# Kernel tuning notes

Hardware: AMD Instinct MI355X
Metric: run time of the kernel (lower is better)

The kernel has to match this reference:

```python
import jax, jax.numpy as jnp
import numpy as np

HID, E, S, L_CAP, EPS = 768, 1536, 128, 512, 1e-5


def _rope_seq(x):
    """RoPE along axis 1. x: [b, n, 2, s]."""
    n, s = x.shape[1], x.shape[-1]
    half = s // 2
    inv_freq = jnp.power(10000.0, -jnp.arange(half, dtype=x.dtype) / half)  # [half]
    sinusoid = jnp.arange(n, dtype=x.dtype)[:, None, None] * inv_freq       # [n,1,half]
    sin, cos = jnp.sin(sinusoid), jnp.cos(sinusoid)
    x1, x2 = jnp.split(x, 2, axis=-1)
    return jnp.concatenate([x1 * cos - x2 * sin, x2 * cos + x1 * sin], axis=-1)


def setup_inputs() -> dict:
    key = jax.random.key(0)
    ks = jax.random.split(key, 6)
    B, L = 32, 512
    return {
        "x": jax.random.normal(ks[0], (B, L, HID), dtype=jnp.float32),
        "ln_gamma": jnp.ones((HID,), jnp.float32),
        "ln_beta": jnp.zeros((HID,), jnp.float32),
        "uv_W": jax.random.normal(ks[1], (HID, 2 * E + S), jnp.float32) * 0.02,
        "uv_b": jnp.zeros((2 * E + S,), jnp.float32),
        "gamma_qk": jax.random.normal(ks[2], (2, S), jnp.float32) * 0.02,
        "beta_qk": jnp.zeros((2, S), jnp.float32),
        "w_rel": jax.random.normal(ks[3], (2 * L_CAP - 1,), jnp.float32) * 0.02,
        "o_W": jax.random.normal(ks[4], (E, HID), jnp.float32) * 0.02,
        "o_b": jnp.zeros((HID,), jnp.float32),
    }


def reference(x, ln_gamma, ln_beta, uv_W, uv_b, gamma_qk, beta_qk, w_rel, o_W, o_b):
    L = x.shape[1]
    shortcut = x
    # LayerNorm
    mu = jnp.mean(x, axis=-1, keepdims=True)
    var = jnp.mean(jnp.square(x - mu), axis=-1, keepdims=True)
    xn = (x - mu) * jax.lax.rsqrt(var + EPS) * ln_gamma + ln_beta
    # uv projection + silu, split into u, v, base
    uv = jax.nn.silu(xn @ uv_W + uv_b)                       # [b, n, 2e+s]
    u, v, base = jnp.split(uv, [E, 2 * E], axis=-1)          # [b,n,e], [b,n,e], [b,n,s]
    # per-head affine then RoPE -> q, k
    base = base[..., None, :] * gamma_qk + beta_qk           # [b, n, 2, s]
    base = _rope_seq(base)
    q, k = base[..., 0, :], base[..., 1, :]
    # relu^2 attention kernel with Toeplitz relative position bias
    qk = jnp.einsum('bnd,bmd->bnm', q, k)
    idx = jnp.arange(L)
    bias = w_rel[idx[None, :] - idx[:, None] + L - 1]        # bias[i,j] = w[j-i+L-1]
    kernel = jnp.square(jax.nn.relu(qk / L + bias))
    # gated value aggregation + output projection + residual
    out = u * jnp.einsum('bnm,bme->bne', kernel, v)
    out = out @ o_W + o_b
    return out + shortcut
```

## Files before the change

kernel.cpp:

```cpp
#include <hip/hip_runtime.h>
#include <hip/hip_bf16.h>
#include <math.h>

typedef __bf16 bf16x8 __attribute__((ext_vector_type(8)));
typedef float f32x4 __attribute__((ext_vector_type(4)));
typedef unsigned short u16x4 __attribute__((ext_vector_type(4)));

#define AS1P const __attribute__((address_space(1))) void*
#define AS3P __attribute__((address_space(3))) void*

__device__ __forceinline__ float b2f(unsigned short h) {
    unsigned int u = ((unsigned int)h) << 16;
    return __builtin_bit_cast(float, u);
}
__device__ __forceinline__ unsigned short f2b(float f) {
    unsigned int u = __builtin_bit_cast(unsigned int, f);
    u += 0x7FFFu + ((u >> 16) & 1u);
    return (unsigned short)(u >> 16);
}
__device__ __forceinline__ float silu(float c) {
    return c * __builtin_amdgcn_rcpf(1.0f + __expf(-c));
}

__global__ __launch_bounds__(256) void k_convT(const float* __restrict__ src,
                                               unsigned short* __restrict__ dst,
                                               int R, int C) {
    __shared__ float tile[32][33];
    int tx = threadIdx.x, ty = threadIdx.y;
    int r0 = blockIdx.y << 5, c0 = blockIdx.x << 5;
#pragma unroll
    for (int i = 0; i < 4; ++i)
        tile[ty + 8 * i][tx] = src[(long long)(r0 + ty + 8 * i) * C + c0 + tx];
    __syncthreads();
#pragma unroll
    for (int i = 0; i < 4; ++i)
        dst[(long long)(c0 + ty + 8 * i) * R + r0 + tx] = f2b(tile[tx][ty + 8 * i]);
}

__global__ __launch_bounds__(256) void k_ln(const float* __restrict__ x,
                                            const float* __restrict__ g,
                                            const float* __restrict__ b,
                                            unsigned short* __restrict__ xn) {
    int row = blockIdx.x;
    int t = threadIdx.x;
    const float* xr = x + (long long)row * 768;
    float v0 = xr[t], v1 = xr[t + 256], v2 = xr[t + 512];
    float s = v0 + v1 + v2;
    float q = v0 * v0 + v1 * v1 + v2 * v2;
#pragma unroll
    for (int off = 32; off > 0; off >>= 1) {
        s += __shfl_xor(s, off);
        q += __shfl_xor(q, off);
    }
    __shared__ float ss[4], sq[4];
    int w = t >> 6;
    if ((t & 63) == 0) { ss[w] = s; sq[w] = q; }
    __syncthreads();
    float S_ = ss[0] + ss[1] + ss[2] + ss[3];
    float Q_ = sq[0] + sq[1] + sq[2] + sq[3];
    float mu = S_ * (1.0f / 768.0f);
    float var = Q_ * (1.0f / 768.0f) - mu * mu;
    float rs = rsqrtf(var + 1e-5f);
    unsigned short* xo = xn + (long long)row * 768;
    xo[t]       = f2b((v0 - mu) * rs * g[t]       + b[t]);
    xo[t + 256] = f2b((v1 - mu) * rs * g[t + 256] + b[t + 256]);
    xo[t + 512] = f2b((v2 - mu) * rs * g[t + 512] + b[t + 512]);
}

__global__ __launch_bounds__(128) void k_rope(const unsigned short* __restrict__ bS,
                                              const float* __restrict__ gqk,
                                              const float* __restrict__ bqk,
                                              unsigned short* __restrict__ q,
                                              unsigned short* __restrict__ k) {
    int row = blockIdx.x;
    int l = row & 511;
    int s = threadIdx.x;
    int j = s & 63;
    int partner = s ^ 64;
    float b0 = b2f(bS[(long long)row * 128 + s]);
    float bp = b2f(bS[(long long)row * 128 + partner]);
    float invf = __expf((float)j * -0.14391156831f);
    float th = (float)l * invf;
    float sn, cs;
    __sincosf(th, &sn, &cs);
    float sign = (s < 64) ? -1.0f : 1.0f;
    float preq  = b0 * gqk[s]           + bqk[s];
    float preqp = bp * gqk[partner]     + bqk[partner];
    q[(long long)row * 128 + s] = f2b(preq * cs + sign * preqp * sn);
    float prek  = b0 * gqk[128 + s]       + bqk[128 + s];
    float prekp = bp * gqk[128 + partner] + bqk[128 + partner];
    k[(long long)row * 128 + s] = f2b(prek * cs + sign * prekp * sn);
}

template <int EPI, int K>
__global__ __launch_bounds__(256) void k_g2(const unsigned short* __restrict__ A,
                                            const unsigned short* __restrict__ B,
                                            const float* __restrict__ p1,
                                            unsigned short* __restrict__ out_) {
    __shared__ __align__(16) unsigned short As[128 * 64];
    __shared__ __align__(16) unsigned short Bs[128 * 64];
    int t = threadIdx.x;
    int w = t >> 6, lane = t & 63;
    int wr = w >> 1, wc = w & 1;
    int bx = blockIdx.x, by = blockIdx.y, bz = blockIdx.z;
    {
        int gx = gridDim.x, gy = gridDim.y;
        int nb = gx * gy * gridDim.z;
        int bid = (bz * gy + by) * gx + bx;
        int s = (bid & 7) * (nb >> 3) + (bid >> 3);
        bx = s % gx;
        by = (s / gx) % gy;
        bz = s / (gx * gy);
    }
    const unsigned short* Ab;
    const unsigned short* Bb;
    if constexpr (EPI == 1) {
        Ab = A + (long long)bz * 512 * 128 + (long long)by * 128 * 128;
        Bb = B + (long long)bz * 512 * 128 + (long long)bx * 128 * 128;
    } else {
        Ab = A + (long long)by * 128 * 768;
        Bb = B;
    }

    f32x4 acc[4][4];
#pragma unroll
    for (int m = 0; m < 4; ++m)
#pragma unroll
        for (int n = 0; n < 4; ++n) acc[m][n] = (f32x4){0.f, 0.f, 0.f, 0.f};

    int rowA = (w << 3) + (lane >> 3);
    int colA = (lane & 7) << 3;

    for (int k0 = 0; k0 < K; k0 += 64) {
#pragma unroll
        for (int i = 0; i < 4; ++i) {
            int r = (i << 5) + rowA;
            __builtin_amdgcn_global_load_lds(
                (AS1P)(Ab + (long long)r * K + k0 + colA),
                (AS3P)(&As[(i << 11) + (w << 9)]), 16, 0, 0);
            __builtin_amdgcn_global_load_lds(
                (AS1P)(Bb + (long long)r * K + k0 + colA),
                (AS3P)(&Bs[(i << 11) + (w << 9)]), 16, 0, 0);
        }
        __syncthreads();
#pragma unroll
        for (int ks = 0; ks < 2; ++ks) {
            bf16x8 af[4], bfr[4];
#pragma unroll
            for (int m = 0; m < 4; ++m)
                af[m] = *(const bf16x8*)&As[((wr << 6) + (m << 4) + (lane & 15)) * 64 +
                                            (ks << 5) + ((lane >> 4) << 3)];
#pragma unroll
            for (int n = 0; n < 4; ++n)
                bfr[n] = *(const bf16x8*)&Bs[((wc << 6) + (n << 4) + (lane & 15)) * 64 +
                                             (ks << 5) + ((lane >> 4) << 3)];
#pragma unroll
            for (int m = 0; m < 4; ++m)
#pragma unroll
                for (int n = 0; n < 4; ++n)
                    acc[m][n] = __builtin_amdgcn_mfma_f32_16x16x32_bf16(bfr[n], af[m],
                                                                        acc[m][n], 0, 0, 0);
        }
        __syncthreads();
    }

    int c15 = lane & 15, qq = lane >> 4;
    int rowb = (by << 7) + (wr << 6) + c15;
    int colb = (bx << 7) + (wc << 6) + (qq << 2);
#pragma unroll
    for (int m = 0; m < 4; ++m) {
#pragma unroll
        for (int n = 0; n < 4; ++n) {
            int grow = rowb + (m << 4);
            int gcol = colb + (n << 4);
            f32x4 a = acc[m][n];
            u16x4 o;
            if constexpr (EPI == 1) {
                int base = gcol - grow + 511;
#pragma unroll
                for (int i = 0; i < 4; ++i) {
                    float val = a[i] * (1.0f / 512.0f) + p1[base + i];
                    val = fmaxf(val, 0.0f);
                    o[i] = f2b(val * val);
                }
                *(u16x4*)(out_ + ((long long)(bz * 512 + grow)) * 512 + gcol) = o;
            } else {
#pragma unroll
                for (int i = 0; i < 4; ++i)
                    o[i] = f2b(silu(a[i] + p1[gcol + i]));
                *(u16x4*)(out_ + (long long)grow * 128 + gcol) = o;
            }
        }
    }
}

__device__ __forceinline__ bf16x8 ldsread(const unsigned short* p) {
    bf16x8 r;
    unsigned int off =
        (unsigned int)(unsigned long long)(__attribute__((address_space(3))) const void*)p;
    asm volatile("ds_read_b128 %0, %1" : "=v"(r) : "v"(off));
    return r;
}
__device__ __forceinline__ void stage_half(const unsigned short* __restrict__ g, int ldk,
                                           unsigned short* lds, int t) {
#pragma unroll
    for (int i = 0; i < 2; ++i) {
        int slot = t + (i << 9);
        int row = slot >> 2;
        int gs = (slot & 3) ^ ((slot >> 3) & 3);
        __builtin_amdgcn_global_load_lds(
            (AS1P)(g + (long long)row * ldk + (gs << 3)),
            (AS3P)(lds + slot * 8), 16, 0, 0);
    }
}

template <bool SWAP, int NT, int NF>
__device__ __forceinline__ void kloop8(const unsigned short* __restrict__ Ab,
                                       const unsigned short* __restrict__ Bb,
                                       unsigned short* As, unsigned short* Bs,
                                       f32x4 (&acc)[8][NF], int tid,
                                       int wr, int wc, int c15, int qq, int gq) {
    constexpr int K = NT * 64;
    stage_half(Ab, K, As + 0, tid);
    stage_half(Bb, K, Bs + 0, tid);
    stage_half(Ab + 32, K, As + 8192, tid);
    stage_half(Bb + 32, K, Bs + 8192, tid);
    stage_half(Ab + 64, K, As + 16384, tid);
    stage_half(Bb + 64, K, Bs + 16384, tid);
    asm volatile("s_waitcnt vmcnt(8)" ::: "memory");
    __builtin_amdgcn_s_barrier();

    bf16x8 bfr[NF], af[4];
    for (int t = 0; t < NT; ++t) {
        const int b = t & 1;
        const unsigned short* A0 = As + b * 16384;
        const unsigned short* B0 = Bs + b * 16384;
#pragma unroll
        for (int p = 0; p < 4; ++p) {
            const int ks = p >> 1, mh = p & 1;
            const unsigned short* At = A0 + ks * 8192;
            const unsigned short* Bt = B0 + ks * 8192;
            if (mh == 0) {
#pragma unroll
                for (int n = 0; n < NF; ++n)
                    bfr[n] = ldsread(Bt + (wc * (NF * 16) + n * 16 + c15) * 32 + gq * 8);
            }
#pragma unroll
            for (int j = 0; j < 4; ++j)
                af[j] = ldsread(At + (wr * 128 + (mh * 4 + j) * 16 + c15) * 32 + gq * 8);
            if (p == 0) {
                if (t + 1 < NT)
                    stage_half(Ab + (t + 1) * 64 + 32, K,
                               As + (((t + 1) & 1) * 2 + 1) * 8192, tid);
            } else if (p == 1) {
                if (t + 1 < NT)
                    stage_half(Bb + (t + 1) * 64 + 32, K,
                               Bs + (((t + 1) & 1) * 2 + 1) * 8192, tid);
            } else if (p == 2) {
                if (t + 2 < NT)
                    stage_half(Ab + (t + 2) * 64, K, As + (b * 2) * 8192, tid);
            } else {
                if (t + 2 < NT)
                    stage_half(Bb + (t + 2) * 64, K, Bs + (b * 2) * 8192, tid);
            }
            __builtin_amdgcn_s_barrier();
            asm volatile("s_waitcnt lgkmcnt(0)" ::: "memory");
            __builtin_amdgcn_sched_barrier(0);
            __builtin_amdgcn_s_setprio(1);
#pragma unroll
            for (int j = 0; j < 4; ++j)
#pragma unroll
                for (int n = 0; n < NF; ++n) {
                    if constexpr (SWAP)
                        acc[mh * 4 + j][n] = __builtin_amdgcn_mfma_f32_16x16x32_bf16(
                            bfr[n], af[j], acc[mh * 4 + j][n], 0, 0, 0);
                    else
                        acc[mh * 4 + j][n] = __builtin_amdgcn_mfma_f32_16x16x32_bf16(
                            af[j], bfr[n], acc[mh * 4 + j][n], 0, 0, 0);
                }
            __builtin_amdgcn_s_setprio(0);
            if (p == 1) {
                if (t < NT - 1)
                    asm volatile("s_waitcnt vmcnt(8)" ::: "memory");
                else
                    asm volatile("s_waitcnt vmcnt(0)" ::: "memory");
            } else if (p == 3) {
                if (t < NT - 2)
                    asm volatile("s_waitcnt vmcnt(8)" ::: "memory");
                else if (t == NT - 2)
                    asm volatile("s_waitcnt vmcnt(4)" ::: "memory");
            }
            __builtin_amdgcn_sched_barrier(0);
            __builtin_amdgcn_s_barrier();
        }
    }
}

template <int EPI, int SWZ, int NT, int NF>
__global__ __launch_bounds__(512, 2) void k8(const unsigned short* __restrict__ A,
                                             const unsigned short* __restrict__ B,
                                             long long strideA, long long strideB,
                                             void* p0, void* p1, void* p2,
                                             const void* p3) {
    constexpr int K = NT * 64;
    __shared__ __align__(16) unsigned short As[2][2][256 * 32];
    __shared__ __align__(16) unsigned short Bs[2][2][256 * 32];
    int tid = threadIdx.x;
    int w = tid >> 6, lane = tid & 63;
    int wr = w >> 2, wc = w & 3;
    int c15 = lane & 15, qq = lane >> 4;
    int gq = qq ^ ((c15 >> 1) & 3);
    int bx = blockIdx.x, by = blockIdx.y, bz = blockIdx.z;
    if constexpr (SWZ == 1) {
        int gx = gridDim.x;
        int nb = gx * gridDim.y;
        int bid = by * gx + bx;
        int s = (bid & 7) * (nb >> 3) + (bid >> 3);
        bx = s % gx;
        by = s / gx;
    } else if constexpr (SWZ == 2) {
        int gx = gridDim.x, gy = gridDim.y;
        int nb = gx * gy * gridDim.z;
        int bid = (bz * gy + by) * gx + bx;
        int s = (bid & 7) * (nb >> 3) + (bid >> 3);
        bx = s % gx;
        by = (s / gx) % gy;
        bz = s / (gx * gy);
    }
    const unsigned short* Ab = A + bz * strideA + (long long)by * 256 * K;
    const unsigned short* Bb = B + bz * strideB + (long long)bx * (NF * 64) * K;

    f32x4 acc[8][NF];
#pragma unroll
    for (int m = 0; m < 8; ++m)
#pragma unroll
        for (int n = 0; n < NF; ++n) acc[m][n] = (f32x4){0.f, 0.f, 0.f, 0.f};

    bool swapped = true;
    if constexpr (EPI == 10) {
        swapped = (bx < 6);
        if (swapped)
            kloop8<true, NT, NF>(Ab, Bb, &As[0][0][0], &Bs[0][0][0], acc, tid, wr, wc, c15, qq, gq);
        else
            kloop8<false, NT, NF>(Ab, Bb, &As[0][0][0], &Bs[0][0][0], acc, tid, wr, wc, c15, qq, gq);
    } else {
        kloop8<true, NT, NF>(Ab, Bb, &As[0][0][0], &Bs[0][0][0], acc, tid, wr, wc, c15, qq, gq);
    }

    if constexpr (EPI == 10) {
        if (swapped) {
            int rowb = by * 256 + wr * 128 + c15;
            int colb = bx * 256 + wc * 64 + (qq << 2);
#pragma unroll
            for (int m = 0; m < 8; ++m) {
#pragma unroll
                for (int n = 0; n < NF; ++n) {
                    int R = rowb + m * 16;
                    int C = colb + n * 16;
                    f32x4 a = acc[m][n];
                    f32x4 bb = *(const f32x4*)((const float*)p3 + C);
                    u16x4 o;
#pragma unroll
                    for (int i = 0; i < 4; ++i) o[i] = f2b(silu(a[i] + bb[i]));
                    *(u16x4*)((unsigned short*)p0 + (long long)R * 1536 + C) = o;
                }
            }
        } else {
            int rowb = by * 256 + wr * 128 + (qq << 2);
            int colb = bx * 256 + wc * 64 + c15;
#pragma unroll
            for (int m = 0; m < 8; ++m) {
#pragma unroll
                for (int n = 0; n < NF; ++n) {
                    int R = rowb + m * 16;
                    int C = colb + n * 16;
                    float bias = ((const float*)p3)[C];
                    f32x4 a = acc[m][n];
                    u16x4 o;
#pragma unroll
                    for (int i = 0; i < 4; ++i) o[i] = f2b(silu(a[i] + bias));
                    int bb2 = R >> 9, mm = R & 511;
                    *(u16x4*)((unsigned short*)p1 +
                              ((long long)bb2 * 1600 + (C - 1536)) * 512 + mm) = o;
                }
            }
        }
    } else if constexpr (EPI == 2) {
        int rowb = by * 256 + wr * 128 + c15;
        int colb = bx * (NF * 64) + wc * (NF * 16) + (qq << 2);
#pragma unroll
        for (int m = 0; m < 8; ++m) {
#pragma unroll
            for (int n = 0; n < NF; ++n) {
                int R = rowb + m * 16;
                int C = colb + n * 16;
                f32x4 a = acc[m][n];
                long long idx = ((long long)(bz * 512 + R)) * 1536 + C;
                u16x4 uu = *(const u16x4*)((const unsigned short*)p1 + idx);
                u16x4 o;
#pragma unroll
                for (int i = 0; i < 4; ++i) o[i] = f2b(a[i] * b2f(uu[i]));
                *(u16x4*)((unsigned short*)p0 + idx) = o;
            }
        }
    } else {
        int rowb = by * 256 + wr * 128 + c15;
        int colb = bx * (NF * 64) + wc * (NF * 16) + (qq << 2);
#pragma unroll
        for (int m = 0; m < 8; ++m) {
#pragma unroll
            for (int n = 0; n < NF; ++n) {
                int R = rowb + m * 16;
                int C = colb + n * 16;
                f32x4 a = acc[m][n];
                long long idx = (long long)R * 768 + C;
                f32x4 xv = *(const f32x4*)((const float*)p2 + idx);
                f32x4 ob = *(const f32x4*)((const float*)p1 + C);
                f32x4 o;
#pragma unroll
                for (int i = 0; i < 4; ++i) o[i] = a[i] + ob[i] + xv[i];
                *(f32x4*)((float*)p0 + idx) = o;
            }
        }
    }
}

extern "C" void kernel_launch(void* const* d_in, const int* in_sizes, int n_in,
                              void* d_out, int out_size, void* d_ws, size_t ws_size,
                              hipStream_t stream) {
    const float* x     = (const float*)d_in[0];
    const float* ln_g  = (const float*)d_in[1];
    const float* ln_b  = (const float*)d_in[2];
    const float* uv_W  = (const float*)d_in[3];
    const float* uv_b  = (const float*)d_in[4];
    const float* g_qk  = (const float*)d_in[5];
    const float* b_qk  = (const float*)d_in[6];
    const float* w_rel = (const float*)d_in[7];
    const float* o_W   = (const float*)d_in[8];
    const float* o_b   = (const float*)d_in[9];
    float* out = (float*)d_out;

    char* ws = (char*)d_ws;
    size_t off = 0;
    auto alloc = [&](size_t bytes) {
        void* p = ws + off;
        off += (bytes + 255) & ~(size_t)255;
        return p;
    };
    unsigned short* uvWT = (unsigned short*)alloc(3200ll * 768 * 2);
    unsigned short* oWT  = (unsigned short*)alloc(832ll * 1536 * 2);
    unsigned short* xn   = (unsigned short*)alloc(16384ll * 768 * 2);
    unsigned short* u    = (unsigned short*)alloc(16384ll * 1536 * 2);
    unsigned short* vT   = (unsigned short*)alloc(32ll * 1600 * 512 * 2);
    unsigned short* bS   = (unsigned short*)alloc(16384ll * 128 * 2);
    unsigned short* q    = (unsigned short*)alloc(32ll * 512 * 128 * 2);
    unsigned short* k    = (unsigned short*)alloc(32ll * 512 * 128 * 2);
    unsigned short* P     = xn;
    unsigned short* gated = u;

    k_convT<<<dim3(100, 24), dim3(32, 8), 0, stream>>>(uv_W, uvWT, 768, 3200);
    k_convT<<<dim3(24, 48), dim3(32, 8), 0, stream>>>(o_W, oWT, 1536, 768);
    k_ln<<<16384, 256, 0, stream>>>(x, ln_g, ln_b, xn);
    k8<10, 1, 12, 4><<<dim3(12, 64), 512, 0, stream>>>(
        xn, uvWT, 0, 0, (void*)u, (void*)vT, nullptr, (const void*)uv_b);
    k_g2<5, 768><<<dim3(1, 128), 256, 0, stream>>>(
        xn, uvWT + 3072ll * 768, uv_b + 3072, bS);
    k_rope<<<16384, 128, 0, stream>>>(bS, g_qk, b_qk, q, k);
    k_g2<1, 128><<<dim3(4, 4, 32), 256, 0, stream>>>(q, k, w_rel, P);
    k8<2, 2, 8, 3><<<dim3(8, 2, 32), 512, 0, stream>>>(
        P, vT, 512ll * 512, 1600ll * 512, (void*)gated, (void*)u, nullptr, nullptr);
    k8<3, 1, 24, 3><<<dim3(4, 64), 512, 0, stream>>>(
        gated, oWT, 0, 0, (void*)out, (void*)o_b, (void*)x, nullptr);
}
```

Baseline: 273.6 us.

## Retile base projection to 64-row blocks and move QK scores onto k8 kernel

The small base-projection GEMM (N=128) is now a dedicated kernel with 64-row tiles, which doubles the grid to 256 blocks for better CU occupancy. The q·k^T relu² score GEMM moves from the 128x128-tile k_g2 kernel to the larger pipelined k8 kernel with a new EPI==1 epilogue that applies the Toeplitz bias. The k buffer is padded by 128 rows, presumably so the k8 loads may read past the end safely. The trade is fewer blocks for the score GEMM (256 vs 512) against the better pipelining in k8.

```diff
diff --git a/kernel.cpp b/kernel.cpp
--- a/kernel.cpp
+++ b/kernel.cpp
@@ -92,70 +92,56 @@
     k[(long long)row * 128 + s] = f2b(prek * cs + sign * prekp * sn);
 }
 
-template <int EPI, int K>
-__global__ __launch_bounds__(256) void k_g2(const unsigned short* __restrict__ A,
+__global__ __launch_bounds__(256) void k_bs(const unsigned short* __restrict__ A,
                                             const unsigned short* __restrict__ B,
-                                            const float* __restrict__ p1,
+                                            const float* __restrict__ bias,
                                             unsigned short* __restrict__ out_) {
-    __shared__ __align__(16) unsigned short As[128 * 64];
+    __shared__ __align__(16) unsigned short As[64 * 64];
     __shared__ __align__(16) unsigned short Bs[128 * 64];
     int t = threadIdx.x;
     int w = t >> 6, lane = t & 63;
     int wr = w >> 1, wc = w & 1;
-    int bx = blockIdx.x, by = blockIdx.y, bz = blockIdx.z;
-    {
-        int gx = gridDim.x, gy = gridDim.y;
-        int nb = gx * gy * gridDim.z;
-        int bid = (bz * gy + by) * gx + bx;
-        int s = (bid & 7) * (nb >> 3) + (bid >> 3);
-        bx = s % gx;
-        by = (s / gx) % gy;
-        bz = s / (gx * gy);
-    }
-    const unsigned short* Ab;
-    const unsigned short* Bb;
-    if constexpr (EPI == 1) {
-        Ab = A + (long long)bz * 512 * 128 + (long long)by * 128 * 128;
-        Bb = B + (long long)bz * 512 * 128 + (long long)bx * 128 * 128;
-    } else {
-        Ab = A + (long long)by * 128 * 768;
-        Bb = B;
-    }
-
-    f32x4 acc[4][4];
-#pragma unroll
-    for (int m = 0; m < 4; ++m)
+    int by = blockIdx.x;
+    const unsigned short* Ab = A + (long long)by * 64 * 768;
+
+    f32x4 acc[2][4];
+#pragma unroll
+    for (int m = 0; m < 2; ++m)
 #pragma unroll
         for (int n = 0; n < 4; ++n) acc[m][n] = (f32x4){0.f, 0.f, 0.f, 0.f};
 
     int rowA = (w << 3) + (lane >> 3);
     int colA = (lane & 7) << 3;
 
-    for (int k0 = 0; k0 < K; k0 += 64) {
+    for (int k0 = 0; k0 < 768; k0 += 64) {
+#pragma unroll
+        for (int i = 0; i < 2; ++i) {
+            int r = (i << 5) + rowA;
+            __builtin_amdgcn_global_load_lds(
+                (AS1P)(Ab + (long long)r * 768 + k0 + colA),
+                (AS3P)(&As[(i << 11) + (w << 9)]), 16, 0, 0);
+        }
 #pragma unroll
         for (int i = 0; i < 4; ++i) {
             int r = (i << 5) + rowA;
             __builtin_amdgcn_global_load_lds(
-                (AS1P)(Ab + (long long)r * K + k0 + colA),
-                (AS3P)(&As[(i << 11) + (w << 9)]), 16, 0, 0);
-            __builtin_amdgcn_global_load_lds(
-                (AS1P)(Bb + (long long)r * K + k0 + colA),
+                (AS1P)(B + (long long)r * 768 + k0 + colA),
                 (AS3P)(&Bs[(i << 11) + (w << 9)]), 16, 0, 0);
         }
         __syncthreads();
 #pragma unroll
         for (int ks = 0; ks < 2; ++ks) {
-            bf16x8 af[4], bfr[4];
-#pragma unroll
-            for (int m = 0; m < 4; ++m)
-                af[m] = *(const bf16x8*)&As[((wr << 6) + (m << 4) + (lane & 15)) * 64 +
+            bf16x8 af[2], bfr[4];
+#pragma unroll
+            for (int m = 0; m < 2; ++m)
+                af[m] = *(const bf16x8*)&As[((wr << 5) + (m << 4) + (lane & 15)) * 64 +
                                             (ks << 5) + ((lane >> 4) << 3)];
 #pragma unroll
             for (int n = 0; n < 4; ++n)
                 bfr[n] = *(const bf16x8*)&Bs[((wc << 6) + (n << 4) + (lane & 15)) * 64 +
                                              (ks << 5) + ((lane >> 4) << 3)];
 #pragma unroll
-            for (int m = 0; m < 4; ++m)
+            for (int m = 0; m < 2; ++m)
 #pragma unroll
                 for (int n = 0; n < 4; ++n)
                     acc[m][n] = __builtin_amdgcn_mfma_f32_16x16x32_bf16(bfr[n], af[m],
@@ -165,31 +151,20 @@
     }
 
     int c15 = lane & 15, qq = lane >> 4;
-    int rowb = (by << 7) + (wr << 6) + c15;
-    int colb = (bx << 7) + (wc << 6) + (qq << 2);
-#pragma unroll
-    for (int m = 0; m < 4; ++m) {
+    int rowb = (by << 6) + (wr << 5) + c15;
+    int colb = (wc << 6) + (qq << 2);
+#pragma unroll
+    for (int m = 0; m < 2; ++m) {
 #pragma unroll
         for (int n = 0; n < 4; ++n) {
             int grow = rowb + (m << 4);
             int gcol = colb + (n << 4);
             f32x4 a = acc[m][n];
             u16x4 o;
-            if constexpr (EPI == 1) {
-                int base = gcol - grow + 511;
-#pragma unroll
-                for (int i = 0; i < 4; ++i) {
-                    float val = a[i] * (1.0f / 512.0f) + p1[base + i];
-                    val = fmaxf(val, 0.0f);
-                    o[i] = f2b(val * val);
-                }
-                *(u16x4*)(out_ + ((long long)(bz * 512 + grow)) * 512 + gcol) = o;
-            } else {
-#pragma unroll
-                for (int i = 0; i < 4; ++i)
-                    o[i] = f2b(silu(a[i] + p1[gcol + i]));
-                *(u16x4*)(out_ + (long long)grow * 128 + gcol) = o;
-            }
+#pragma unroll
+            for (int i = 0; i < 4; ++i)
+                o[i] = f2b(silu(a[i] + bias[gcol + i]));
+            *(u16x4*)(out_ + (long long)grow * 128 + gcol) = o;
         }
     }
 }
@@ -385,6 +360,28 @@
                 }
             }
         }
+    } else if constexpr (EPI == 1) {
+        const float* wrel = (const float*)p1;
+        int rowb = by * 256 + wr * 128 + c15;
+        int colb = bx * (NF * 64) + wc * (NF * 16) + (qq << 2);
+#pragma unroll
+        for (int m = 0; m < 8; ++m) {
+#pragma unroll
+            for (int n = 0; n < NF; ++n) {
+                int R = rowb + m * 16;
+                int C = colb + n * 16;
+                f32x4 a = acc[m][n];
+                int base = C - R + 511;
+                u16x4 o;
+#pragma unroll
+                for (int i = 0; i < 4; ++i) {
+                    float val = a[i] * (1.0f / 512.0f) + wrel[base + i];
+                    val = fmaxf(val, 0.0f);
+                    o[i] = f2b(val * val);
+                }
+                *(u16x4*)((unsigned short*)p0 + ((long long)(bz * 512 + R)) * 512 + C) = o;
+            }
+        }
     } else if constexpr (EPI == 2) {
         int rowb = by * 256 + wr * 128 + c15;
         int colb = bx * (NF * 64) + wc * (NF * 16) + (qq << 2);
@@ -454,7 +451,7 @@
     unsigned short* vT   = (unsigned short*)alloc(32ll * 1600 * 512 * 2);
     unsigned short* bS   = (unsigned short*)alloc(16384ll * 128 * 2);
     unsigned short* q    = (unsigned short*)alloc(32ll * 512 * 128 * 2);
-    unsigned short* k    = (unsigned short*)alloc(32ll * 512 * 128 * 2);
+    unsigned short* k    = (unsigned short*)alloc((32ll * 512 + 128) * 128 * 2);
     unsigned short* P     = xn;
     unsigned short* gated = u;
 
@@ -463,10 +460,10 @@
     k_ln<<<16384, 256, 0, stream>>>(x, ln_g, ln_b, xn);
     k8<10, 1, 12, 4><<<dim3(12, 64), 512, 0, stream>>>(
         xn, uvWT, 0, 0, (void*)u, (void*)vT, nullptr, (const void*)uv_b);
-    k_g2<5, 768><<<dim3(1, 128), 256, 0, stream>>>(
-        xn, uvWT + 3072ll * 768, uv_b + 3072, bS);
+    k_bs<<<256, 256, 0, stream>>>(xn, uvWT + 3072ll * 768, uv_b + 3072, bS);
     k_rope<<<16384, 128, 0, stream>>>(bS, g_qk, b_qk, q, k);
-    k_g2<1, 128><<<dim3(4, 4, 32), 256, 0, stream>>>(q, k, w_rel, P);
+    k8<1, 2, 2, 2><<<dim3(4, 2, 32), 512, 0, stream>>>(
+        q, k, 512ll * 128, 512ll * 128, (void*)P, (void*)w_rel, nullptr, nullptr);
     k8<2, 2, 8, 3><<<dim3(8, 2, 32), 512, 0, stream>>>(
         P, vT, 512ll * 512, 1600ll * 512, (void*)gated, (void*)u, nullptr, nullptr);
     k8<3, 1, 24, 3><<<dim3(4, 64), 512, 0, stream>>>(
```

Result: faster. 268.1 us (-2.0%).
